# Performance work log

Measured on AMD Instinct MI355X. Metric: run time of the kernel, lower is better.

The kernel has to match this reference:

```python
import jax, jax.numpy as jnp
import numpy as np

N0, N1, N2, N3, N4, C = 65536, 16384, 4096, 1024, 256, 256


def _linear_params(key, fan_in, fan_out):
    kw, kb = jax.random.split(key)
    lim = 1.0 / np.sqrt(fan_in)
    W = jax.random.uniform(kw, (fan_in, fan_out), minval=-lim, maxval=lim, dtype=jnp.float32)
    b = jax.random.uniform(kb, (fan_out,), minval=-lim, maxval=lim, dtype=jnp.float32)
    return W, b


def setup_inputs() -> dict:
    key = jax.random.key(0)
    ks = jax.random.split(key, 20)
    inp = {
        'xyz0': jax.random.normal(ks[0], (N0, 3), dtype=jnp.float32),
        'idx0': jax.random.randint(ks[1], (N0,), 0, N1),
        'idx1': jax.random.randint(ks[2], (N1,), 0, N0),
        'idx2': jax.random.randint(ks[3], (N2,), 0, N0),
        'idx3': jax.random.randint(ks[4], (N3,), 0, N0),
        'idx4': jax.random.randint(ks[5], (N4,), 0, N0),
    }
    names = ['W_all', 'b_all', 'W4', 'b4', 'W3', 'b3', 'W2', 'b2', 'W1', 'b1', 'W0', 'b0']
    for i in range(6):
        W, b = _linear_params(ks[6 + i], 3, C)
        inp[names[2 * i]] = W
        inp[names[2 * i + 1]] = b
    pnames = ['P4', 'pb4', 'P3', 'pb3', 'P2', 'pb2', 'P1', 'pb1', 'P0', 'pb0']
    for i in range(5):
        W, b = _linear_params(ks[12 + i], 2 * C, C)
        inp[pnames[2 * i]] = W
        inp[pnames[2 * i + 1]] = b
    return inp


def _nn1(xyz, new_xyz):
    # global 1-NN (single batch segment): argmin of squared distance
    d = (jnp.sum(new_xyz ** 2, -1, keepdims=True)
         - 2.0 * new_xyz @ xyz.T
         + jnp.sum(xyz ** 2, -1))  # [M, N]
    return jnp.argmin(d, axis=1)


def _fwd(xyz0, idx0, idx1, idx2, idx3, idx4,
         W_all, b_all, W4, b4, W3, b3, W2, b2, W1, b1, W0, b0,
         P4, pb4, P3, pb3, P2, pb2, P1, pb1, P0, pb0):
    xyz4 = xyz0[idx4]
    xyz3 = xyz0[idx3]
    xyz2 = xyz0[idx2]
    xyz1 = xyz0[idx1]
    f0 = xyz0 @ W_all + b_all          # [N0, C]
    f1, f2, f3, f4 = f0[:N1], f0[:N2], f0[:N3], f0[:N4]
    # level 4: global max pooling as class token (single-batch scatter-amax)
    cls4 = jnp.max(f4, axis=0, keepdims=True)  # [1, C], broadcasts over N4
    f4_nei = cls4 + (xyz4 @ W4 + b4)
    pe4 = jnp.concatenate([f4_nei, f4], axis=-1) @ P4 + pb4
    # level 3
    k34 = _nn1(xyz4, xyz3)
    f3_nei = pe4[k34] + ((xyz3 - xyz4[k34]) @ W3 + b3)
    pe3 = jnp.concatenate([f3_nei, f3], axis=-1) @ P3 + pb3
    # level 2
    k23 = _nn1(xyz3, xyz2)
    f2_nei = pe3[k23] + ((xyz2 - xyz3[k23]) @ W2 + b2)
    pe2 = jnp.concatenate([f2_nei, f2], axis=-1) @ P2 + pb2
    # level 1
    k12 = _nn1(xyz2, xyz1)
    f1_nei = pe2[k12] + ((xyz1 - xyz2[k12]) @ W1 + b1)
    pe1 = jnp.concatenate([f1_nei, f1], axis=-1) @ P1 + pb1
    # level 0: precomputed indices into level 1
    f0_nei = pe1[idx0] + ((xyz0 - xyz1[idx0]) @ W0 + b0)
    pe0 = jnp.concatenate([f0_nei, f0], axis=-1) @ P0 + pb0
    return (pe4, pe3, pe2, pe1, pe0)


def reference(xyz0, idx0, idx1, idx2, idx3, idx4,
              W_all, b_all, W4, b4, W3, b3, W2, b2, W1, b1, W0, b0,
              P4, pb4, P3, pb3, P2, pb2, P1, pb1, P0, pb0):
    return _fwd(xyz0, idx0, idx1, idx2, idx3, idx4,
                W_all, b_all, W4, b4, W3, b3, W2, b2, W1, b1, W0, b0,
                P4, pb4, P3, pb3, P2, pb2, P1, pb1, P0, pb0)
```

## Files before the change

### kernel.cpp

```cpp
#include <hip/hip_runtime.h>
#include <hip/hip_bf16.h>


typedef __hip_bfloat16 bf16;
typedef unsigned short ushort_t;
typedef __attribute__((ext_vector_type(8))) short short8;
typedef __attribute__((ext_vector_type(4))) float float4v;

#define cN0 65536
#define cN1 16384
#define cN2 4096
#define cN3 1024
#define cN4 256

__device__ __forceinline__ float b2f(bf16 v) { return __bfloat162float(v); }

__device__ __forceinline__ ushort_t f2b(float v) {
    union { float f; unsigned u; } x; x.f = v;
    unsigned r = x.u + 0x7FFF + ((x.u >> 16) & 1);
    return (ushort_t)(r >> 16);
}

__global__ void detect_kernel(const unsigned short* __restrict__ raw, int* __restrict__ flag) {
    __shared__ int bad;
    if (threadIdx.x == 0) bad = 0;
    __syncthreads();
    for (int i = threadIdx.x; i < 1024; i += 256) {
        int e = (raw[i] >> 7) & 0xFF;
        if (e >= 138) atomicOr(&bad, 1);
    }
    __syncthreads();
    if (threadIdx.x == 0) flag[0] = bad ? 1 : 0;
}

struct CanonArgs { const void* src[23]; };

__global__ void canon_kernel(CanonArgs a, const int* __restrict__ flag, float* __restrict__ dst) {
    const int sizes[23] = {196608, 768, 256,
                           768, 256, 768, 256, 768, 256, 768, 256, 768, 256,
                           131072, 256, 131072, 256, 131072, 256, 131072, 256, 131072, 256};
    int fp32 = flag[0];
    int gid = blockIdx.x * 256 + threadIdx.x;
    int off = 0;
#pragma unroll
    for (int s = 0; s < 23; ++s) {
        int n = sizes[s];
        if (gid >= off && gid < off + n) {
            int local = gid - off;
            float v = fp32 ? ((const float*)a.src[s])[local]
                           : b2f(((const bf16*)a.src[s])[local]);
            dst[gid] = v;
        }
        off += n;
    }
}

__global__ void prep_kernel(const float* __restrict__ Pbase, const float* __restrict__ Wbase,
                            const float* __restrict__ Wallf, const float* __restrict__ ballf,
                            const float* __restrict__ xyzf,
                            ushort_t* __restrict__ PTb,
                            float* __restrict__ M1, float* __restrict__ M2,
                            float* __restrict__ cbuf) {
    __shared__ __align__(16) char smem[16640];
    int bidx = blockIdx.x;
    int tid = threadIdx.x;

    if (bidx < 80) {
        int level = bidx >> 4;
        int kb = (bidx >> 2) & 3;
        int nb = bidx & 3;
        const float* P = Pbase + (size_t)level * 131328;
        ushort_t* PT = PTb + (size_t)level * 65536;
        float (*tile)[65] = (float (*)[65])smem;
        int tx = tid & 63, ty = tid >> 6;
        for (int r = ty; r < 64; r += 4)
            tile[r][tx] = P[(size_t)(kb * 64 + r) * 256 + nb * 64 + tx];
        __syncthreads();
        for (int r = ty; r < 64; r += 4)
            PT[(size_t)(nb * 64 + r) * 256 + kb * 64 + tx] = f2b(tile[tx][r]);
        return;
    }

    int L = (bidx - 80) >> 3;
    int tb = (bidx - 80) & 7;
    const float* P = Pbase + (size_t)L * 131328;
    const float* W = Wbase + (size_t)L * 1024;
    const float* b = W + 768;
    const float* pb = P + 131072;

    float* cls4f = (float*)smem;
    float* red = (float*)(smem + 1024);
    float* px = (float*)(smem + 1024 + 7168);
    float* py = px + 256;
    float* pz = py + 256;

    if (L == 0) {
        px[tid] = xyzf[3 * tid + 0];
        py[tid] = xyzf[3 * tid + 1];
        pz[tid] = xyzf[3 * tid + 2];
        __syncthreads();
        float w0 = Wallf[tid], w1 = Wallf[256 + tid], w2 = Wallf[512 + tid];
        float bb = ballf[tid];
        float best = -3.402823466e38f;
        for (int i = 0; i < 256; ++i) {
            float v = fmaf(pz[i], w2, fmaf(py[i], w1, px[i] * w0)) + bb;
            best = fmaxf(best, v);
        }
        cls4f[tid] = best;
        __syncthreads();
    }

    int j = tid & 31;
    int slice = tid >> 5;
    int col = tb * 32 + j;

    float m10 = 0.f, m11 = 0.f, m12 = 0.f, m20 = 0.f, m21 = 0.f, m22 = 0.f, cc = 0.f;
#pragma unroll 4
    for (int i = 0; i < 32; ++i) {
        int c = slice * 32 + i;
        float pt = P[(size_t)c * 256 + col];
        float pbot = P[(size_t)(256 + c) * 256 + col];
        m10 = fmaf(W[c], pt, m10);
        m11 = fmaf(W[256 + c], pt, m11);
        m12 = fmaf(W[512 + c], pt, m12);
        m20 = fmaf(Wallf[c], pbot, m20);
        m21 = fmaf(Wallf[256 + c], pbot, m21);
        m22 = fmaf(Wallf[512 + c], pbot, m22);
        cc = fmaf(b[c], pt, cc);
        cc = fmaf(ballf[c], pbot, cc);
        if (L == 0) cc = fmaf(cls4f[c], pt, cc);
    }

    red[0 * 256 + tid] = m10; red[1 * 256 + tid] = m11; red[2 * 256 + tid] = m12;
    red[3 * 256 + tid] = m20; red[4 * 256 + tid] = m21; red[5 * 256 + tid] = m22;
    red[6 * 256 + tid] = cc;
    __syncthreads();
    if (tid < 32) {
        float v[7];
#pragma unroll
        for (int q = 0; q < 7; ++q) {
            float s = red[q * 256 + tid];
#pragma unroll
            for (int sl = 1; sl < 8; ++sl) s += red[q * 256 + sl * 32 + tid];
            v[q] = s;
        }
        M1[(size_t)L * 768 + col] = v[0];
        M1[(size_t)L * 768 + 256 + col] = v[1];
        M1[(size_t)L * 768 + 512 + col] = v[2];
        M2[(size_t)L * 768 + col] = v[3];
        M2[(size_t)L * 768 + 256 + col] = v[4];
        M2[(size_t)L * 768 + 512 + col] = v[5];
        cbuf[(size_t)L * 256 + col] = v[6] + pb[col];
    }
}

__device__ __forceinline__ void nn_body(const float* __restrict__ xyzf,
                                        const int* __restrict__ idxQ,
                                        const int* __restrict__ idxR, int nR,
                                        int* __restrict__ outK, int blk,
                                        float4* ref4, float* redD, int* redI) {
    int tid = threadIdx.x;
    int part = tid >> 6;
    int q = blk * 64 + (tid & 63);
    int qi = idxQ[q];
    float qx = xyzf[3 * qi + 0];
    float qy = xyzf[3 * qi + 1];
    float qz = xyzf[3 * qi + 2];
    float q2 = (qx * qx + qy * qy) + qz * qz;
    float best = 3.402823466e38f;
    int bi = 0;
    for (int base = 0; base < nR; base += 1024) {
        int nt = min(1024, nR - base);
        __syncthreads();
        for (int t = tid; t < nt; t += 256) {
            int ri = idxR[base + t];
            float x = xyzf[3 * ri + 0];
            float y = xyzf[3 * ri + 1];
            float z = xyzf[3 * ri + 2];
            ref4[t] = make_float4(x, y, z, (x * x + y * y) + z * z);
        }
        __syncthreads();
        int seg = nt >> 2;
        int s0 = part * seg;
        for (int t = 0; t < seg; ++t) {
            float4 rp = ref4[s0 + t];
            float dot = (qx * rp.x + qy * rp.y) + qz * rp.z;
            float d = (q2 - 2.0f * dot) + rp.w;
            if (d < best) { best = d; bi = base + s0 + t; }
        }
    }
    redD[tid] = best;
    redI[tid] = bi;
    __syncthreads();
    if (part == 0) {
#pragma unroll
        for (int p = 1; p < 4; ++p) {
            float d = redD[tid + p * 64];
            int i2 = redI[tid + p * 64];
            if (d < best || (d == best && i2 < bi)) { best = d; bi = i2; }
        }
        outK[q] = bi;
    }
}

__global__ void nn_merged(const float* __restrict__ xyzf,
                          const int* __restrict__ idx1, const int* __restrict__ idx2,
                          const int* __restrict__ idx3, const int* __restrict__ idx4,
                          int* __restrict__ k34, int* __restrict__ k23,
                          int* __restrict__ k12) {
    __shared__ __align__(16) float4 ref4[1024];
    __shared__ float redD[256];
    __shared__ int redI[256];
    int b = blockIdx.x;
    if (b < 16)       nn_body(xyzf, idx3, idx4, cN4, k34, b, ref4, redD, redI);
    else if (b < 80)  nn_body(xyzf, idx2, idx3, cN3, k23, b - 16, ref4, redD, redI);
    else              nn_body(xyzf, idx1, idx2, cN2, k12, b - 80, ref4, redD, redI);
}

__global__ void pe4_kernel(const float* __restrict__ xyzf, const int* __restrict__ idx4,
                           const float* __restrict__ M1, const float* __restrict__ M2,
                           const float* __restrict__ cbuf, const int* __restrict__ flag,
                           void* __restrict__ outv, ushort_t* __restrict__ peB) {
    int row = blockIdx.x;
    int n = threadIdx.x;
    int qi = idx4[row];
    float qx = xyzf[3 * qi + 0], qy = xyzf[3 * qi + 1], qz = xyzf[3 * qi + 2];
    float xx = xyzf[3 * row + 0], yy = xyzf[3 * row + 1], zz = xyzf[3 * row + 2];
    float v = cbuf[n];
    v = fmaf(qx, M1[n], v);
    v = fmaf(qy, M1[256 + n], v);
    v = fmaf(qz, M1[512 + n], v);
    v = fmaf(xx, M2[n], v);
    v = fmaf(yy, M2[256 + n], v);
    v = fmaf(zz, M2[512 + n], v);
    size_t idx = (size_t)row * 256 + n;
    if (flag[0]) ((float*)outv)[idx] = v;
    else         ((bf16*)outv)[idx] = __float2bfloat16(v);
    peB[idx] = f2b(v);
}

__global__ __launch_bounds__(256, 2) void level_mfma(
    const float* __restrict__ xyzf,
    const ushort_t* __restrict__ peB_prev,
    const int* __restrict__ kmap,
    const int* __restrict__ idxQ,
    const int* __restrict__ idxR,
    const float* __restrict__ M1, const float* __restrict__ M2,
    const float* __restrict__ cvec,
    const ushort_t* __restrict__ PT,
    const int* __restrict__ flag, void* __restrict__ outv, size_t out_off,
    ushort_t* __restrict__ peB_out) {
    __shared__ float m1l[768], m2l[768], cl[256];
    __shared__ float rowD[64][3], rowX[64][3];
    __shared__ int rowK[64];
    __shared__ __align__(16) ushort_t A_lds[64 * 264];

    int tid = threadIdx.x;
    int row0 = blockIdx.x * 64;
    int fp32out = flag[0];

    for (int i = tid; i < 768; i += 256) { m1l[i] = M1[i]; m2l[i] = M2[i]; }
    cl[tid] = cvec[tid];
    if (tid < 64) {
        int r = tid, row = row0 + r;
        float xx = xyzf[3 * row + 0];
        float yy = xyzf[3 * row + 1];
        float zz = xyzf[3 * row + 2];
        rowX[r][0] = xx; rowX[r][1] = yy; rowX[r][2] = zz;
        int k = kmap[row];
        rowK[r] = k;
        float qx = xx, qy = yy, qz = zz;
        if (idxQ) {
            int qi = idxQ[row];
            qx = xyzf[3 * qi + 0];
            qy = xyzf[3 * qi + 1];
            qz = xyzf[3 * qi + 2];
        }
        int ri = idxR[k];
        float rx = xyzf[3 * ri + 0];
        float ry = xyzf[3 * ri + 1];
        float rz = xyzf[3 * ri + 2];
        rowD[r][0] = qx - rx; rowD[r][1] = qy - ry; rowD[r][2] = qz - rz;
    }
    __syncthreads();

#pragma unroll
    for (int it = 0; it < 8; ++it) {
        int lin = it * 256 + tid;
        int r = lin >> 5, ch = lin & 31;
        *(uint4*)&A_lds[r * 264 + ch * 8] =
            *(const uint4*)(peB_prev + (size_t)rowK[r] * 256 + ch * 8);
    }
    __syncthreads();

    int wave = tid >> 6;
    int lane = tid & 63;
    int quad = lane >> 4;
    int l16 = lane & 15;
    int wc = wave * 64;

    const ushort_t* bbase[4];
#pragma unroll
    for (int nt = 0; nt < 4; ++nt)
        bbase[nt] = PT + (size_t)(wc + nt * 16 + l16) * 256 + quad * 8;

    float4v acc[4][4];
#pragma unroll
    for (int mt = 0; mt < 4; ++mt)
#pragma unroll
        for (int nt = 0; nt < 4; ++nt) acc[mt][nt] = (float4v){0.f, 0.f, 0.f, 0.f};

#pragma unroll
    for (int kt = 0; kt < 8; ++kt) {
        int c0 = kt * 32;
        short8 afr[4], bfr[4];
#pragma unroll
        for (int nt = 0; nt < 4; ++nt)
            bfr[nt] = *(const short8*)(bbase[nt] + c0);
#pragma unroll
        for (int mt = 0; mt < 4; ++mt)
            afr[mt] = *(const short8*)&A_lds[(mt * 16 + l16) * 264 + c0 + quad * 8];
#pragma unroll
        for (int mt = 0; mt < 4; ++mt)
#pragma unroll
            for (int nt = 0; nt < 4; ++nt)
                acc[mt][nt] = __builtin_amdgcn_mfma_f32_16x16x32_bf16(
                    afr[mt], bfr[nt], acc[mt][nt], 0, 0, 0);
    }

#pragma unroll
    for (int mt = 0; mt < 4; ++mt) {
#pragma unroll
        for (int reg = 0; reg < 4; ++reg) {
            int rl = mt * 16 + quad * 4 + reg;
            float d0 = rowD[rl][0], d1 = rowD[rl][1], d2 = rowD[rl][2];
            float x0 = rowX[rl][0], x1 = rowX[rl][1], x2 = rowX[rl][2];
            int row = row0 + rl;
#pragma unroll
            for (int nt = 0; nt < 4; ++nt) {
                int col = wc + nt * 16 + l16;
                float v = acc[mt][nt][reg] + cl[col];
                v = fmaf(d0, m1l[col], v);
                v = fmaf(d1, m1l[256 + col], v);
                v = fmaf(d2, m1l[512 + col], v);
                v = fmaf(x0, m2l[col], v);
                v = fmaf(x1, m2l[256 + col], v);
                v = fmaf(x2, m2l[512 + col], v);
                size_t idx = (size_t)row * 256 + col;
                if (fp32out) ((float*)outv)[out_off + idx] = v;
                else         ((bf16*)outv)[out_off + idx] = __float2bfloat16(v);
                if (peB_out) peB_out[idx] = f2b(v);
            }
        }
    }
}

extern "C" void kernel_launch(void* const* d_in, const int* in_sizes, int n_in,
                              void* d_out, int out_size, void* d_ws, size_t ws_size,
                              hipStream_t stream) {
    const int* idx0 = (const int*)d_in[1];
    const int* idx1 = (const int*)d_in[2];
    const int* idx2 = (const int*)d_in[3];
    const int* idx3 = (const int*)d_in[4];
    const int* idx4 = (const int*)d_in[5];

    float* ws = (float*)d_ws;
    int* flag = (int*)ws;
    float* p = ws + 64;
    float* xyzf = p;  p += 196608;
    float* Wallf = p; p += 768;
    float* ballf = p; p += 256;
    float* Wf0 = p;   p += 5 * 1024;
    float* Pf0 = p;   p += 5 * 131328;
    float* M1buf = p; p += 5 * 768;
    float* M2buf = p; p += 5 * 768;
    float* cbuf = p;  p += 5 * 256;
    int* k34 = (int*)p; p += 1024;
    int* k23 = (int*)p; p += 4096;
    int* k12 = (int*)p; p += 16384;
    ushort_t* pe4B = (ushort_t*)p; p += 32768;
    ushort_t* pe3B = (ushort_t*)p; p += 131072;
    ushort_t* pe2B = (ushort_t*)p; p += 524288;
    ushort_t* pe1B = (ushort_t*)p; p += 2097152;
    ushort_t* PTb = (ushort_t*)p;

    detect_kernel<<<1, 256, 0, stream>>>((const unsigned short*)d_in[0], flag);

    CanonArgs ca;
    ca.src[0] = d_in[0];
    ca.src[1] = d_in[6];
    ca.src[2] = d_in[7];
    for (int i = 0; i < 10; ++i) ca.src[3 + i] = d_in[8 + i];
    for (int i = 0; i < 10; ++i) ca.src[13 + i] = d_in[18 + i];
    canon_kernel<<<3357, 256, 0, stream>>>(ca, flag, ws + 64);

    prep_kernel<<<120, 256, 0, stream>>>(Pf0, Wf0, Wallf, ballf, xyzf,
                                         PTb, M1buf, M2buf, cbuf);
    nn_merged<<<336, 256, 0, stream>>>(xyzf, idx1, idx2, idx3, idx4, k34, k23, k12);

    const size_t o4 = 0;
    const size_t o3 = (size_t)cN4 * 256;
    const size_t o2 = o3 + (size_t)cN3 * 256;
    const size_t o1 = o2 + (size_t)cN2 * 256;
    const size_t o0 = o1 + (size_t)cN1 * 256;

    pe4_kernel<<<cN4, 256, 0, stream>>>(xyzf, idx4, M1buf, M2buf, cbuf, flag, d_out, pe4B);

    level_mfma<<<cN3 / 64, 256, 0, stream>>>(
        xyzf, pe4B, k34, idx3, idx4, M1buf + 768, M2buf + 768, cbuf + 256,
        PTb + 1 * 65536, flag, d_out, o3, pe3B);
    level_mfma<<<cN2 / 64, 256, 0, stream>>>(
        xyzf, pe3B, k23, idx2, idx3, M1buf + 2 * 768, M2buf + 2 * 768, cbuf + 2 * 256,
        PTb + 2 * 65536, flag, d_out, o2, pe2B);
    level_mfma<<<cN1 / 64, 256, 0, stream>>>(
        xyzf, pe2B, k12, idx1, idx2, M1buf + 3 * 768, M2buf + 3 * 768, cbuf + 3 * 256,
        PTb + 3 * 65536, flag, d_out, o1, pe1B);
    level_mfma<<<cN0 / 64, 256, 0, stream>>>(
        xyzf, pe1B, idx0, nullptr, idx1, M1buf + 4 * 768, M2buf + 4 * 768, cbuf + 4 * 256,
        PTb + 4 * 65536, flag, d_out, o0, nullptr);
}
```

Baseline: 290.1 us.

## Fuse prep/NN into one kernel and chain all levels in a persistent kernel

Removes the separate detect and canonicalize kernels by reading raw inputs (bf16 or fp32) directly with inline conversion. Merges prep, transpose and nearest-neighbour search into a single 512-thread launch. Collapses pe4 and the four per-level MFMA launches into one levels_kernel that uses atomic done-counters for cross-level dependencies, with pe4 computed inline. The goal is to cut launch overhead and the global round trip of the canonicalized copies. In exchange it adds spin-wait synchronization that depends on block scheduling order and co-residency.

After: 569.1 us. 96.2% more time.

```diff
diff --git a/kernel.cpp b/kernel.cpp
--- a/kernel.cpp
+++ b/kernel.cpp
@@ -13,7 +13,20 @@
 #define cN3 1024
 #define cN4 256
 
-__device__ __forceinline__ float b2f(bf16 v) { return __bfloat162float(v); }
+__device__ __forceinline__ float bits2f(ushort_t u) {
+    union { unsigned u; float f; } x; x.u = ((unsigned)u) << 16; return x.f;
+}
+__device__ __forceinline__ float ldf(const void* raw, int fp32, int i) {
+    return fp32 ? ((const float*)raw)[i] : bits2f(((const ushort_t*)raw)[i]);
+}
+__device__ __forceinline__ float3 ld3(const void* raw, int fp32, int i) {
+    if (fp32) {
+        const float* f = (const float*)raw + 3 * i;
+        return make_float3(f[0], f[1], f[2]);
+    }
+    const ushort_t* u = (const ushort_t*)raw + 3 * i;
+    return make_float3(bits2f(u[0]), bits2f(u[1]), bits2f(u[2]));
+}
 
 __device__ __forceinline__ ushort_t f2b(float v) {
     union { float f; unsigned u; } x; x.f = v;
@@ -21,140 +34,15 @@
     return (ushort_t)(r >> 16);
 }
 
-__global__ void detect_kernel(const unsigned short* __restrict__ raw, int* __restrict__ flag) {
-    __shared__ int bad;
-    if (threadIdx.x == 0) bad = 0;
-    __syncthreads();
-    for (int i = threadIdx.x; i < 1024; i += 256) {
-        int e = (raw[i] >> 7) & 0xFF;
-        if (e >= 138) atomicOr(&bad, 1);
-    }
-    __syncthreads();
-    if (threadIdx.x == 0) flag[0] = bad ? 1 : 0;
-}
-
-struct CanonArgs { const void* src[23]; };
-
-__global__ void canon_kernel(CanonArgs a, const int* __restrict__ flag, float* __restrict__ dst) {
-    const int sizes[23] = {196608, 768, 256,
-                           768, 256, 768, 256, 768, 256, 768, 256, 768, 256,
-                           131072, 256, 131072, 256, 131072, 256, 131072, 256, 131072, 256};
-    int fp32 = flag[0];
-    int gid = blockIdx.x * 256 + threadIdx.x;
-    int off = 0;
-#pragma unroll
-    for (int s = 0; s < 23; ++s) {
-        int n = sizes[s];
-        if (gid >= off && gid < off + n) {
-            int local = gid - off;
-            float v = fp32 ? ((const float*)a.src[s])[local]
-                           : b2f(((const bf16*)a.src[s])[local]);
-            dst[gid] = v;
-        }
-        off += n;
-    }
-}
-
-__global__ void prep_kernel(const float* __restrict__ Pbase, const float* __restrict__ Wbase,
-                            const float* __restrict__ Wallf, const float* __restrict__ ballf,
-                            const float* __restrict__ xyzf,
-                            ushort_t* __restrict__ PTb,
-                            float* __restrict__ M1, float* __restrict__ M2,
-                            float* __restrict__ cbuf) {
-    __shared__ __align__(16) char smem[16640];
-    int bidx = blockIdx.x;
-    int tid = threadIdx.x;
-
-    if (bidx < 80) {
-        int level = bidx >> 4;
-        int kb = (bidx >> 2) & 3;
-        int nb = bidx & 3;
-        const float* P = Pbase + (size_t)level * 131328;
-        ushort_t* PT = PTb + (size_t)level * 65536;
-        float (*tile)[65] = (float (*)[65])smem;
-        int tx = tid & 63, ty = tid >> 6;
-        for (int r = ty; r < 64; r += 4)
-            tile[r][tx] = P[(size_t)(kb * 64 + r) * 256 + nb * 64 + tx];
-        __syncthreads();
-        for (int r = ty; r < 64; r += 4)
-            PT[(size_t)(nb * 64 + r) * 256 + kb * 64 + tx] = f2b(tile[tx][r]);
-        return;
-    }
-
-    int L = (bidx - 80) >> 3;
-    int tb = (bidx - 80) & 7;
-    const float* P = Pbase + (size_t)L * 131328;
-    const float* W = Wbase + (size_t)L * 1024;
-    const float* b = W + 768;
-    const float* pb = P + 131072;
-
-    float* cls4f = (float*)smem;
-    float* red = (float*)(smem + 1024);
-    float* px = (float*)(smem + 1024 + 7168);
-    float* py = px + 256;
-    float* pz = py + 256;
-
-    if (L == 0) {
-        px[tid] = xyzf[3 * tid + 0];
-        py[tid] = xyzf[3 * tid + 1];
-        pz[tid] = xyzf[3 * tid + 2];
-        __syncthreads();
-        float w0 = Wallf[tid], w1 = Wallf[256 + tid], w2 = Wallf[512 + tid];
-        float bb = ballf[tid];
-        float best = -3.402823466e38f;
-        for (int i = 0; i < 256; ++i) {
-            float v = fmaf(pz[i], w2, fmaf(py[i], w1, px[i] * w0)) + bb;
-            best = fmaxf(best, v);
-        }
-        cls4f[tid] = best;
-        __syncthreads();
-    }
-
-    int j = tid & 31;
-    int slice = tid >> 5;
-    int col = tb * 32 + j;
-
-    float m10 = 0.f, m11 = 0.f, m12 = 0.f, m20 = 0.f, m21 = 0.f, m22 = 0.f, cc = 0.f;
-#pragma unroll 4
-    for (int i = 0; i < 32; ++i) {
-        int c = slice * 32 + i;
-        float pt = P[(size_t)c * 256 + col];
-        float pbot = P[(size_t)(256 + c) * 256 + col];
-        m10 = fmaf(W[c], pt, m10);
-        m11 = fmaf(W[256 + c], pt, m11);
-        m12 = fmaf(W[512 + c], pt, m12);
-        m20 = fmaf(Wallf[c], pbot, m20);
-        m21 = fmaf(Wallf[256 + c], pbot, m21);
-        m22 = fmaf(Wallf[512 + c], pbot, m22);
-        cc = fmaf(b[c], pt, cc);
-        cc = fmaf(ballf[c], pbot, cc);
-        if (L == 0) cc = fmaf(cls4f[c], pt, cc);
-    }
-
-    red[0 * 256 + tid] = m10; red[1 * 256 + tid] = m11; red[2 * 256 + tid] = m12;
-    red[3 * 256 + tid] = m20; red[4 * 256 + tid] = m21; red[5 * 256 + tid] = m22;
-    red[6 * 256 + tid] = cc;
-    __syncthreads();
-    if (tid < 32) {
-        float v[7];
-#pragma unroll
-        for (int q = 0; q < 7; ++q) {
-            float s = red[q * 256 + tid];
-#pragma unroll
-            for (int sl = 1; sl < 8; ++sl) s += red[q * 256 + sl * 32 + tid];
-            v[q] = s;
-        }
-        M1[(size_t)L * 768 + col] = v[0];
-        M1[(size_t)L * 768 + 256 + col] = v[1];
-        M1[(size_t)L * 768 + 512 + col] = v[2];
-        M2[(size_t)L * 768 + col] = v[3];
-        M2[(size_t)L * 768 + 256 + col] = v[4];
-        M2[(size_t)L * 768 + 512 + col] = v[5];
-        cbuf[(size_t)L * 256 + col] = v[6] + pb[col];
-    }
-}
-
-__device__ __forceinline__ void nn_body(const float* __restrict__ xyzf,
+struct RawArgs {
+    const void* xyz;
+    const void* Wall; const void* ball;
+    const void* W[5]; const void* bb[5];
+    const void* P[5]; const void* pb[5];
+};
+
+
+__device__ __forceinline__ void nn_body(const void* xyzr, int fp32,
                                         const int* __restrict__ idxQ,
                                         const int* __restrict__ idxR, int nR,
                                         int* __restrict__ outK, int blk,
@@ -163,24 +51,22 @@
     int part = tid >> 6;
     int q = blk * 64 + (tid & 63);
     int qi = idxQ[q];
-    float qx = xyzf[3 * qi + 0];
-    float qy = xyzf[3 * qi + 1];
-    float qz = xyzf[3 * qi + 2];
+    float3 qv = ld3(xyzr, fp32, qi);
+    float qx = qv.x, qy = qv.y, qz = qv.z;
     float q2 = (qx * qx + qy * qy) + qz * qz;
     float best = 3.402823466e38f;
     int bi = 0;
     for (int base = 0; base < nR; base += 1024) {
         int nt = min(1024, nR - base);
         __syncthreads();
-        for (int t = tid; t < nt; t += 256) {
+        for (int t = tid; t < nt; t += 512) {
             int ri = idxR[base + t];
-            float x = xyzf[3 * ri + 0];
-            float y = xyzf[3 * ri + 1];
-            float z = xyzf[3 * ri + 2];
-            ref4[t] = make_float4(x, y, z, (x * x + y * y) + z * z);
-        }
-        __syncthreads();
-        int seg = nt >> 2;
+            float3 r3 = ld3(xyzr, fp32, ri);
+            ref4[t] = make_float4(r3.x, r3.y, r3.z,
+                                  (r3.x * r3.x + r3.y * r3.y) + r3.z * r3.z);
+        }
+        __syncthreads();
+        int seg = nt >> 3;
         int s0 = part * seg;
         for (int t = 0; t < seg; ++t) {
             float4 rp = ref4[s0 + t];
@@ -194,7 +80,7 @@
     __syncthreads();
     if (part == 0) {
 #pragma unroll
-        for (int p = 1; p < 4; ++p) {
+        for (int p = 1; p < 8; ++p) {
             float d = redD[tid + p * 64];
             int i2 = redI[tid + p * 64];
             if (d < best || (d == best && i2 < bi)) { best = d; bi = i2; }
@@ -203,95 +89,246 @@
     }
 }
 
-__global__ void nn_merged(const float* __restrict__ xyzf,
-                          const int* __restrict__ idx1, const int* __restrict__ idx2,
-                          const int* __restrict__ idx3, const int* __restrict__ idx4,
-                          int* __restrict__ k34, int* __restrict__ k23,
-                          int* __restrict__ k12) {
-    __shared__ __align__(16) float4 ref4[1024];
-    __shared__ float redD[256];
-    __shared__ int redI[256];
+__global__ void prep_nn_kernel(RawArgs ra,
+                               const int* __restrict__ idx1, const int* __restrict__ idx2,
+                               const int* __restrict__ idx3, const int* __restrict__ idx4,
+                               ushort_t* __restrict__ PTb,
+                               float* __restrict__ M1, float* __restrict__ M2,
+                               float* __restrict__ cbuf,
+                               int* __restrict__ k34, int* __restrict__ k23,
+                               int* __restrict__ k12,
+                               int* __restrict__ flag, int* __restrict__ cnt) {
+    __shared__ __align__(16) char smem[20608];
+    __shared__ int sbad;
     int b = blockIdx.x;
-    if (b < 16)       nn_body(xyzf, idx3, idx4, cN4, k34, b, ref4, redD, redI);
-    else if (b < 80)  nn_body(xyzf, idx2, idx3, cN3, k23, b - 16, ref4, redD, redI);
-    else              nn_body(xyzf, idx1, idx2, cN2, k12, b - 80, ref4, redD, redI);
-}
-
-__global__ void pe4_kernel(const float* __restrict__ xyzf, const int* __restrict__ idx4,
-                           const float* __restrict__ M1, const float* __restrict__ M2,
-                           const float* __restrict__ cbuf, const int* __restrict__ flag,
-                           void* __restrict__ outv, ushort_t* __restrict__ peB) {
-    int row = blockIdx.x;
-    int n = threadIdx.x;
-    int qi = idx4[row];
-    float qx = xyzf[3 * qi + 0], qy = xyzf[3 * qi + 1], qz = xyzf[3 * qi + 2];
-    float xx = xyzf[3 * row + 0], yy = xyzf[3 * row + 1], zz = xyzf[3 * row + 2];
-    float v = cbuf[n];
-    v = fmaf(qx, M1[n], v);
-    v = fmaf(qy, M1[256 + n], v);
-    v = fmaf(qz, M1[512 + n], v);
-    v = fmaf(xx, M2[n], v);
-    v = fmaf(yy, M2[256 + n], v);
-    v = fmaf(zz, M2[512 + n], v);
-    size_t idx = (size_t)row * 256 + n;
-    if (flag[0]) ((float*)outv)[idx] = v;
-    else         ((bf16*)outv)[idx] = __float2bfloat16(v);
-    peB[idx] = f2b(v);
-}
-
-__global__ __launch_bounds__(256, 2) void level_mfma(
-    const float* __restrict__ xyzf,
-    const ushort_t* __restrict__ peB_prev,
-    const int* __restrict__ kmap,
-    const int* __restrict__ idxQ,
-    const int* __restrict__ idxR,
-    const float* __restrict__ M1, const float* __restrict__ M2,
-    const float* __restrict__ cvec,
-    const ushort_t* __restrict__ PT,
-    const int* __restrict__ flag, void* __restrict__ outv, size_t out_off,
-    ushort_t* __restrict__ peB_out) {
+    int tid = threadIdx.x;
+
+    if (tid == 0) sbad = 0;
+    __syncthreads();
+    {
+        const ushort_t* raw0 = (const ushort_t*)ra.xyz;
+        for (int i = tid; i < 1024; i += 512) {
+            int e = (raw0[i] >> 7) & 0xFF;
+            if (e >= 138) atomicOr(&sbad, 1);
+        }
+    }
+    __syncthreads();
+    int fp32 = sbad ? 1 : 0;
+    if (b == 0 && tid == 0) {
+        flag[0] = fp32;
+        cnt[0] = 0; cnt[1] = 0; cnt[2] = 0;
+    }
+
+    if (b < 64) {
+        int level = 1 + (b >> 4);
+        int kb = (b >> 2) & 3;
+        int nb = b & 3;
+        const void* P = ra.P[level];
+        ushort_t* PT = PTb + (size_t)level * 65536;
+        float (*tile)[65] = (float (*)[65])smem;
+        int tx = tid & 63, ty = tid >> 6;
+        for (int r = ty; r < 64; r += 8)
+            tile[r][tx] = ldf(P, fp32, (kb * 64 + r) * 256 + nb * 64 + tx);
+        __syncthreads();
+        for (int r = ty; r < 64; r += 8)
+            PT[(size_t)(nb * 64 + r) * 256 + kb * 64 + tx] = f2b(tile[tx][r]);
+        return;
+    }
+
+    if (b < 104) {
+        int L = (b - 64) >> 3;
+        int tb = (b - 64) & 7;
+        const void* P = ra.P[L];
+        const void* W = ra.W[L];
+        const void* bvec = ra.bb[L];
+        const void* pb = ra.pb[L];
+        float* cls4f = (float*)smem;
+        float* red = (float*)(smem + 1024);
+        float* px = (float*)(smem + 1024 + 7168);
+        float* py = px + 256;
+        float* pz = py + 256;
+
+        if (L == 0) {
+            if (tid < 256) {
+                float3 x = ld3(ra.xyz, fp32, tid);
+                px[tid] = x.x; py[tid] = x.y; pz[tid] = x.z;
+            }
+            __syncthreads();
+            if (tid < 256) {
+                float w0 = ldf(ra.Wall, fp32, tid);
+                float w1 = ldf(ra.Wall, fp32, 256 + tid);
+                float w2 = ldf(ra.Wall, fp32, 512 + tid);
+                float bbv = ldf(ra.ball, fp32, tid);
+                float best = -3.402823466e38f;
+                for (int i = 0; i < 256; ++i) {
+                    float v = fmaf(pz[i], w2, fmaf(py[i], w1, px[i] * w0)) + bbv;
+                    best = fmaxf(best, v);
+                }
+                cls4f[tid] = best;
+            }
+            __syncthreads();
+        }
+
+        if (tid < 256) {
+            int j = tid & 31;
+            int slice = tid >> 5;
+            int col = tb * 32 + j;
+            float m10 = 0.f, m11 = 0.f, m12 = 0.f, m20 = 0.f, m21 = 0.f, m22 = 0.f, cc = 0.f;
+#pragma unroll 4
+            for (int i = 0; i < 32; ++i) {
+                int c = slice * 32 + i;
+                float pt = ldf(P, fp32, c * 256 + col);
+                float pbot = ldf(P, fp32, (256 + c) * 256 + col);
+                m10 = fmaf(ldf(W, fp32, c), pt, m10);
+                m11 = fmaf(ldf(W, fp32, 256 + c), pt, m11);
+                m12 = fmaf(ldf(W, fp32, 512 + c), pt, m12);
+                m20 = fmaf(ldf(ra.Wall, fp32, c), pbot, m20);
+                m21 = fmaf(ldf(ra.Wall, fp32, 256 + c), pbot, m21);
+                m22 = fmaf(ldf(ra.Wall, fp32, 512 + c), pbot, m22);
+                cc = fmaf(ldf(bvec, fp32, c), pt, cc);
+                cc = fmaf(ldf(ra.ball, fp32, c), pbot, cc);
+                if (L == 0) cc = fmaf(cls4f[c], pt, cc);
+            }
+            red[0 * 256 + tid] = m10; red[1 * 256 + tid] = m11; red[2 * 256 + tid] = m12;
+            red[3 * 256 + tid] = m20; red[4 * 256 + tid] = m21; red[5 * 256 + tid] = m22;
+            red[6 * 256 + tid] = cc;
+        }
+        __syncthreads();
+        if (tid < 32) {
+            int col = tb * 32 + tid;
+            float v[7];
+#pragma unroll
+            for (int q = 0; q < 7; ++q) {
+                float s = red[q * 256 + tid];
+#pragma unroll
+                for (int sl = 1; sl < 8; ++sl) s += red[q * 256 + sl * 32 + tid];
+                v[q] = s;
+            }
+            M1[(size_t)L * 768 + col] = v[0];
+            M1[(size_t)L * 768 + 256 + col] = v[1];
+            M1[(size_t)L * 768 + 512 + col] = v[2];
+            M2[(size_t)L * 768 + col] = v[3];
+            M2[(size_t)L * 768 + 256 + col] = v[4];
+            M2[(size_t)L * 768 + 512 + col] = v[5];
+            cbuf[(size_t)L * 256 + col] = v[6] + ldf(pb, fp32, col);
+        }
+        return;
+    }
+
+    int blk = b - 104;
+    float4* ref4 = (float4*)smem;
+    float* redD = (float*)(smem + 16384);
+    int* redI = (int*)(smem + 18432);
+    if (blk < 16)       nn_body(ra.xyz, fp32, idx3, idx4, cN4, k34, blk, ref4, redD, redI);
+    else if (blk < 80)  nn_body(ra.xyz, fp32, idx2, idx3, cN3, k23, blk - 16, ref4, redD, redI);
+    else                nn_body(ra.xyz, fp32, idx1, idx2, cN2, k12, blk - 80, ref4, redD, redI);
+}
+
+__global__ __launch_bounds__(256, 2) void levels_kernel(
+    const void* __restrict__ xyz_raw,
+    const int* __restrict__ idx0, const int* __restrict__ idx1,
+    const int* __restrict__ idx2, const int* __restrict__ idx3,
+    const int* __restrict__ idx4,
+    const int* __restrict__ k34, const int* __restrict__ k23,
+    const int* __restrict__ k12,
+    const float* __restrict__ M1buf, const float* __restrict__ M2buf,
+    const float* __restrict__ cbuf,
+    const ushort_t* __restrict__ PTb,
+    const int* __restrict__ flag, void* __restrict__ outv,
+    ushort_t* __restrict__ pe3B, ushort_t* __restrict__ pe2B,
+    ushort_t* __restrict__ pe1B,
+    int* __restrict__ cnt) {
     __shared__ float m1l[768], m2l[768], cl[256];
-    __shared__ float rowD[64][3], rowX[64][3];
+    __shared__ float rowD[64][3], rowX[64][3], refQ[64][3], refK[64][3];
     __shared__ int rowK[64];
     __shared__ __align__(16) ushort_t A_lds[64 * 264];
 
+    int b = blockIdx.x;
     int tid = threadIdx.x;
-    int row0 = blockIdx.x * 64;
-    int fp32out = flag[0];
+    int fp32 = flag[0];
+
+    const size_t o4 = 0;
+    const size_t o3 = 65536;
+    const size_t o2 = 327680;
+    const size_t o1 = 1376256;
+    const size_t o0 = 5570560;
+
+    if (b >= 16 && b < 20) {
+        int rows0 = (b - 16) * 64;
+        if (tid < 64) {
+            int k = rows0 + tid;
+            float3 q = ld3(xyz_raw, fp32, idx4[k]);
+            float3 x = ld3(xyz_raw, fp32, k);
+            refQ[tid][0] = q.x; refQ[tid][1] = q.y; refQ[tid][2] = q.z;
+            refK[tid][0] = x.x; refK[tid][1] = x.y; refK[tid][2] = x.z;
+        }
+        __syncthreads();
+        float cc = cbuf[tid];
+        float a0 = M1buf[tid], a1 = M1buf[256 + tid], a2 = M1buf[512 + tid];
+        float b0 = M2buf[tid], b1 = M2buf[256 + tid], b2 = M2buf[512 + tid];
+        for (int r = 0; r < 64; ++r) {
+            float v = cc;
+            v = fmaf(refQ[r][0], a0, v);
+            v = fmaf(refQ[r][1], a1, v);
+            v = fmaf(refQ[r][2], a2, v);
+            v = fmaf(refK[r][0], b0, v);
+            v = fmaf(refK[r][1], b1, v);
+            v = fmaf(refK[r][2], b2, v);
+            size_t idx = o4 + (size_t)(rows0 + r) * 256 + tid;
+            if (fp32) ((float*)outv)[idx] = v;
+            else      ((bf16*)outv)[idx] = __float2bfloat16(v);
+        }
+        return;
+    }
+
+    int level, t0, tcnt;
+    const int* kmap; const int* idxQ; const int* idxR;
+    const ushort_t* peprev; ushort_t* peout;
+    size_t ooff;
+    const float* M1; const float* M2; const float* cv;
+    const ushort_t* PT;
+    int* waitc = nullptr; int target = 0; int* donec = nullptr;
+
+    if (b < 16) {
+        level = 3; t0 = b; tcnt = 1;
+        kmap = k34; idxQ = idx3; idxR = idx4;
+        peprev = nullptr; peout = pe3B; ooff = o3;
+        M1 = M1buf + 768; M2 = M2buf + 768; cv = cbuf + 256;
+        PT = PTb + 1 * 65536;
+        donec = cnt + 0;
+    } else if (b < 84) {
+        level = 2; t0 = b - 20; tcnt = 1;
+        kmap = k23; idxQ = idx2; idxR = idx3;
+        peprev = pe3B; peout = pe2B; ooff = o2;
+        M1 = M1buf + 1536; M2 = M2buf + 1536; cv = cbuf + 512;
+        PT = PTb + 2 * 65536;
+        waitc = cnt + 0; target = 16; donec = cnt + 1;
+    } else if (b < 212) {
+        level = 1; t0 = (b - 84) * 2; tcnt = 2;
+        kmap = k12; idxQ = idx1; idxR = idx2;
+        peprev = pe2B; peout = pe1B; ooff = o1;
+        M1 = M1buf + 2304; M2 = M2buf + 2304; cv = cbuf + 768;
+        PT = PTb + 3 * 65536;
+        waitc = cnt + 1; target = 64; donec = cnt + 2;
+    } else {
+        level = 0; t0 = (b - 212) * 4; tcnt = 4;
+        kmap = idx0; idxQ = nullptr; idxR = idx1;
+        peprev = pe1B; peout = nullptr; ooff = o0;
+        M1 = M1buf + 3072; M2 = M2buf + 3072; cv = cbuf + 1024;
+        PT = PTb + 4 * 65536;
+        waitc = cnt + 2; target = 128; donec = nullptr;
+    }
 
     for (int i = tid; i < 768; i += 256) { m1l[i] = M1[i]; m2l[i] = M2[i]; }
-    cl[tid] = cvec[tid];
-    if (tid < 64) {
-        int r = tid, row = row0 + r;
-        float xx = xyzf[3 * row + 0];
-        float yy = xyzf[3 * row + 1];
-        float zz = xyzf[3 * row + 2];
-        rowX[r][0] = xx; rowX[r][1] = yy; rowX[r][2] = zz;
-        int k = kmap[row];
-        rowK[r] = k;
-        float qx = xx, qy = yy, qz = zz;
-        if (idxQ) {
-            int qi = idxQ[row];
-            qx = xyzf[3 * qi + 0];
-            qy = xyzf[3 * qi + 1];
-            qz = xyzf[3 * qi + 2];
-        }
-        int ri = idxR[k];
-        float rx = xyzf[3 * ri + 0];
-        float ry = xyzf[3 * ri + 1];
-        float rz = xyzf[3 * ri + 2];
-        rowD[r][0] = qx - rx; rowD[r][1] = qy - ry; rowD[r][2] = qz - rz;
-    }
-    __syncthreads();
-
-#pragma unroll
-    for (int it = 0; it < 8; ++it) {
-        int lin = it * 256 + tid;
-        int r = lin >> 5, ch = lin & 31;
-        *(uint4*)&A_lds[r * 264 + ch * 8] =
-            *(const uint4*)(peB_prev + (size_t)rowK[r] * 256 + ch * 8);
-    }
-    __syncthreads();
+    cl[tid] = cv[tid];
+
+    if (waitc) {
+        if (tid == 0) {
+            while (__hip_atomic_load(waitc, __ATOMIC_ACQUIRE, __HIP_MEMORY_SCOPE_AGENT) < target)
+                __builtin_amdgcn_s_sleep(8);
+        }
+        __syncthreads();
+    }
 
     int wave = tid >> 6;
     int lane = tid & 63;
@@ -304,54 +341,112 @@
     for (int nt = 0; nt < 4; ++nt)
         bbase[nt] = PT + (size_t)(wc + nt * 16 + l16) * 256 + quad * 8;
 
-    float4v acc[4][4];
-#pragma unroll
-    for (int mt = 0; mt < 4; ++mt)
-#pragma unroll
-        for (int nt = 0; nt < 4; ++nt) acc[mt][nt] = (float4v){0.f, 0.f, 0.f, 0.f};
-
-#pragma unroll
-    for (int kt = 0; kt < 8; ++kt) {
-        int c0 = kt * 32;
-        short8 afr[4], bfr[4];
-#pragma unroll
-        for (int nt = 0; nt < 4; ++nt)
-            bfr[nt] = *(const short8*)(bbase[nt] + c0);
+    for (int tt = 0; tt < tcnt; ++tt) {
+        int row0 = (t0 + tt) * 64;
+        __syncthreads();
+        if (tid < 64) {
+            int r = tid, row = row0 + r;
+            float3 x = ld3(xyz_raw, fp32, row);
+            rowX[r][0] = x.x; rowX[r][1] = x.y; rowX[r][2] = x.z;
+            int k = kmap[row];
+            rowK[r] = k;
+            float qx = x.x, qy = x.y, qz = x.z;
+            if (idxQ) {
+                float3 q = ld3(xyz_raw, fp32, idxQ[row]);
+                qx = q.x; qy = q.y; qz = q.z;
+            }
+            int ri = idxR[k];
+            float3 rr = ld3(xyz_raw, fp32, ri);
+            rowD[r][0] = qx - rr.x; rowD[r][1] = qy - rr.y; rowD[r][2] = qz - rr.z;
+            if (level == 3) {
+                refQ[r][0] = rr.x; refQ[r][1] = rr.y; refQ[r][2] = rr.z;
+                float3 kk = ld3(xyz_raw, fp32, k);
+                refK[r][0] = kk.x; refK[r][1] = kk.y; refK[r][2] = kk.z;
+            }
+        }
+        __syncthreads();
+
+        if (level == 3) {
+            float cc = cbuf[tid];
+            float a0 = M1buf[tid], a1 = M1buf[256 + tid], a2 = M1buf[512 + tid];
+            float b0 = M2buf[tid], b1 = M2buf[256 + tid], b2 = M2buf[512 + tid];
+            for (int r = 0; r < 64; ++r) {
+                float v = cc;
+                v = fmaf(refQ[r][0], a0, v);
+                v = fmaf(refQ[r][1], a1, v);
+                v = fmaf(refQ[r][2], a2, v);
+                v = fmaf(refK[r][0], b0, v);
+                v = fmaf(refK[r][1], b1, v);
+                v = fmaf(refK[r][2], b2, v);
+                A_lds[r * 264 + tid] = f2b(v);
+            }
+        } else {
+#pragma unroll
+            for (int it = 0; it < 8; ++it) {
+                int lin = it * 256 + tid;
+                int r = lin >> 5, ch = lin & 31;
+                *(uint4*)&A_lds[r * 264 + ch * 8] =
+                    *(const uint4*)(peprev + (size_t)rowK[r] * 256 + ch * 8);
+            }
+        }
+        __syncthreads();
+
+        float4v acc[4][4];
 #pragma unroll
         for (int mt = 0; mt < 4; ++mt)
-            afr[mt] = *(const short8*)&A_lds[(mt * 16 + l16) * 264 + c0 + quad * 8];
-#pragma unroll
-        for (int mt = 0; mt < 4; ++mt)
+#pragma unroll
+            for (int nt = 0; nt < 4; ++nt) acc[mt][nt] = (float4v){0.f, 0.f, 0.f, 0.f};
+
+#pragma unroll
+        for (int kt = 0; kt < 8; ++kt) {
+            int c0 = kt * 32;
+            short8 afr[4], bfr[4];
 #pragma unroll
             for (int nt = 0; nt < 4; ++nt)
-                acc[mt][nt] = __builtin_amdgcn_mfma_f32_16x16x32_bf16(
-                    afr[mt], bfr[nt], acc[mt][nt], 0, 0, 0);
-    }
-
-#pragma unroll
-    for (int mt = 0; mt < 4; ++mt) {
-#pragma unroll
-        for (int reg = 0; reg < 4; ++reg) {
-            int rl = mt * 16 + quad * 4 + reg;
-            float d0 = rowD[rl][0], d1 = rowD[rl][1], d2 = rowD[rl][2];
-            float x0 = rowX[rl][0], x1 = rowX[rl][1], x2 = rowX[rl][2];
-            int row = row0 + rl;
-#pragma unroll
-            for (int nt = 0; nt < 4; ++nt) {
-                int col = wc + nt * 16 + l16;
-                float v = acc[mt][nt][reg] + cl[col];
-                v = fmaf(d0, m1l[col], v);
-                v = fmaf(d1, m1l[256 + col], v);
-                v = fmaf(d2, m1l[512 + col], v);
-                v = fmaf(x0, m2l[col], v);
-                v = fmaf(x1, m2l[256 + col], v);
-                v = fmaf(x2, m2l[512 + col], v);
-                size_t idx = (size_t)row * 256 + col;
-                if (fp32out) ((float*)outv)[out_off + idx] = v;
-                else         ((bf16*)outv)[out_off + idx] = __float2bfloat16(v);
-                if (peB_out) peB_out[idx] = f2b(v);
-            }
-        }
+                bfr[nt] = *(const short8*)(bbase[nt] + c0);
+#pragma unroll
+            for (int mt = 0; mt < 4; ++mt)
+                afr[mt] = *(const short8*)&A_lds[(mt * 16 + l16) * 264 + c0 + quad * 8];
+#pragma unroll
+            for (int mt = 0; mt < 4; ++mt)
+#pragma unroll
+                for (int nt = 0; nt < 4; ++nt)
+                    acc[mt][nt] = __builtin_amdgcn_mfma_f32_16x16x32_bf16(
+                        afr[mt], bfr[nt], acc[mt][nt], 0, 0, 0);
+        }
+
+#pragma unroll
+        for (int mt = 0; mt < 4; ++mt) {
+#pragma unroll
+            for (int reg = 0; reg < 4; ++reg) {
+                int rl = mt * 16 + quad * 4 + reg;
+                float d0 = rowD[rl][0], d1 = rowD[rl][1], d2 = rowD[rl][2];
+                float x0 = rowX[rl][0], x1 = rowX[rl][1], x2 = rowX[rl][2];
+                int row = row0 + rl;
+#pragma unroll
+                for (int nt = 0; nt < 4; ++nt) {
+                    int col = wc + nt * 16 + l16;
+                    float v = acc[mt][nt][reg] + cl[col];
+                    v = fmaf(d0, m1l[col], v);
+                    v = fmaf(d1, m1l[256 + col], v);
+                    v = fmaf(d2, m1l[512 + col], v);
+                    v = fmaf(x0, m2l[col], v);
+                    v = fmaf(x1, m2l[256 + col], v);
+                    v = fmaf(x2, m2l[512 + col], v);
+                    size_t idx = (size_t)row * 256 + col;
+                    if (fp32) ((float*)outv)[ooff + idx] = v;
+                    else      ((bf16*)outv)[ooff + idx] = __float2bfloat16(v);
+                    if (peout) peout[idx] = f2b(v);
+                }
+            }
+        }
+    }
+
+    if (donec) {
+        __threadfence();
+        __syncthreads();
+        if (tid == 0)
+            __hip_atomic_fetch_add(donec, 1, __ATOMIC_RELEASE, __HIP_MEMORY_SCOPE_AGENT);
     }
 }
 
@@ -366,56 +461,36 @@
 
     float* ws = (float*)d_ws;
     int* flag = (int*)ws;
+    int* cnt = (int*)ws + 1;
     float* p = ws + 64;
-    float* xyzf = p;  p += 196608;
-    float* Wallf = p; p += 768;
-    float* ballf = p; p += 256;
-    float* Wf0 = p;   p += 5 * 1024;
-    float* Pf0 = p;   p += 5 * 131328;
     float* M1buf = p; p += 5 * 768;
     float* M2buf = p; p += 5 * 768;
     float* cbuf = p;  p += 5 * 256;
     int* k34 = (int*)p; p += 1024;
     int* k23 = (int*)p; p += 4096;
     int* k12 = (int*)p; p += 16384;
-    ushort_t* pe4B = (ushort_t*)p; p += 32768;
     ushort_t* pe3B = (ushort_t*)p; p += 131072;
     ushort_t* pe2B = (ushort_t*)p; p += 524288;
     ushort_t* pe1B = (ushort_t*)p; p += 2097152;
     ushort_t* PTb = (ushort_t*)p;
 
-    detect_kernel<<<1, 256, 0, stream>>>((const unsigned short*)d_in[0], flag);
-
-    CanonArgs ca;
-    ca.src[0] = d_in[0];
-    ca.src[1] = d_in[6];
-    ca.src[2] = d_in[7];
-    for (int i = 0; i < 10; ++i) ca.src[3 + i] = d_in[8 + i];
-    for (int i = 0; i < 10; ++i) ca.src[13 + i] = d_in[18 + i];
-    canon_kernel<<<3357, 256, 0, stream>>>(ca, flag, ws + 64);
-
-    prep_kernel<<<120, 256, 0, stream>>>(Pf0, Wf0, Wallf, ballf, xyzf,
-                                         PTb, M1buf, M2buf, cbuf);
-    nn_merged<<<336, 256, 0, stream>>>(xyzf, idx1, idx2, idx3, idx4, k34, k23, k12);
-
-    const size_t o4 = 0;
-    const size_t o3 = (size_t)cN4 * 256;
-    const size_t o2 = o3 + (size_t)cN3 * 256;
-    const size_t o1 = o2 + (size_t)cN2 * 256;
-    const size_t o0 = o1 + (size_t)cN1 * 256;
-
-    pe4_kernel<<<cN4, 256, 0, stream>>>(xyzf, idx4, M1buf, M2buf, cbuf, flag, d_out, pe4B);
-
-    level_mfma<<<cN3 / 64, 256, 0, stream>>>(
-        xyzf, pe4B, k34, idx3, idx4, M1buf + 768, M2buf + 768, cbuf + 256,
-        PTb + 1 * 65536, flag, d_out, o3, pe3B);
-    level_mfma<<<cN2 / 64, 256, 0, stream>>>(
-        xyzf, pe3B, k23, idx2, idx3, M1buf + 2 * 768, M2buf + 2 * 768, cbuf + 2 * 256,
-        PTb + 2 * 65536, flag, d_out, o2, pe2B);
-    level_mfma<<<cN1 / 64, 256, 0, stream>>>(
-        xyzf, pe2B, k12, idx1, idx2, M1buf + 3 * 768, M2buf + 3 * 768, cbuf + 3 * 256,
-        PTb + 3 * 65536, flag, d_out, o1, pe1B);
-    level_mfma<<<cN0 / 64, 256, 0, stream>>>(
-        xyzf, pe1B, idx0, nullptr, idx1, M1buf + 4 * 768, M2buf + 4 * 768, cbuf + 4 * 256,
-        PTb + 4 * 65536, flag, d_out, o0, nullptr);
-}
+    RawArgs ra;
+    ra.xyz = d_in[0];
+    ra.Wall = d_in[6];
+    ra.ball = d_in[7];
+    for (int i = 0; i < 5; ++i) {
+        ra.W[i] = d_in[8 + 2 * i];
+        ra.bb[i] = d_in[9 + 2 * i];
+        ra.P[i] = d_in[18 + 2 * i];
+        ra.pb[i] = d_in[19 + 2 * i];
+    }
+
+    prep_nn_kernel<<<440, 512, 0, stream>>>(ra, idx1, idx2, idx3, idx4,
+                                            PTb, M1buf, M2buf, cbuf,
+                                            k34, k23, k12, flag, cnt);
+
+    levels_kernel<<<468, 256, 0, stream>>>(
+        d_in[0], idx0, idx1, idx2, idx3, idx4,
+        k34, k23, k12, M1buf, M2buf, cbuf, PTb,
+        flag, d_out, pe3B, pe2B, pe1B, cnt);
+}
```
